# Optimization experiments

Measured on AMD Instinct MI355X. Metric: run time of the kernel, lower is better.

Reference implementation:

```python
import math
import jax, jax.numpy as jnp
import numpy as np

B, T, QDIM, ADIM = 256, 2048, 1024, 128
DC, DK = 8, 21          # dynamic channels / kernel
SC, SK = 8, 21          # static channels / kernel
PL, ALPHA, BETA = 11, 0.1, 0.9


def _betabinom_pmf_flipped(n, a, b, length):
    lg = np.vectorize(math.lgamma)
    k = np.arange(length, dtype=np.float64)
    logp = (lg(n + 1.0) - lg(k + 1.0) - lg(n - k + 1.0)
            + lg(k + a) + lg(n - k + b) - lg(n + a + b)
            - (lg(a) + lg(b) - lg(a + b)))
    return np.exp(logp)[::-1].copy()  # .flip(0) as in the torch buffer


def setup_inputs() -> dict:
    key = jax.random.key(0)
    ks = jax.random.split(key, 10)

    def lin(k, shape, fan_in):
        return (jax.random.normal(k, shape, jnp.float32) / np.sqrt(fan_in)).astype(jnp.float32)

    query = jax.random.normal(ks[0], (B, QDIM), jnp.float32)
    # previous-step alignment: a valid probability distribution over T
    alignment_pre = jax.nn.softmax(2.0 * jax.random.normal(ks[1], (B, T), jnp.float32), axis=1)

    P = jnp.asarray(_betabinom_pmf_flipped(PL - 1, ALPHA, BETA, PL), jnp.float32)
    W_w = lin(ks[2], (ADIM, QDIM), QDIM)
    W_b = jnp.zeros((ADIM,), jnp.float32)
    V_w = lin(ks[3], (DC * DK, ADIM), ADIM)
    F_w = lin(ks[4], (SC, 1, SK), SK)        # Conv1d(1, SC, SK) weight
    U_w = lin(ks[5], (ADIM, SC), SC)
    T_w = lin(ks[6], (ADIM, DC), DC)
    T_b = jnp.zeros((ADIM,), jnp.float32)
    v_w = lin(ks[7], (1, ADIM), ADIM)
    return {"query": query, "alignment_pre": alignment_pre, "P": P,
            "W_w": W_w, "W_b": W_b, "V_w": V_w, "F_w": F_w,
            "U_w": U_w, "T_w": T_w, "T_b": T_b, "v_w": v_w}


def reference(query, alignment_pre, P, W_w, W_b, V_w, F_w, U_w, T_w, T_b, v_w):
    b, t = alignment_pre.shape
    pad = (DK - 1) // 2  # == PL - 1 == 10, shared by all three convs
    x_pad = jnp.pad(alignment_pre, ((0, 0), (pad, pad)))
    # sliding windows (cross-correlation layout): windows[b, t, k] = x_pad[b, t + k]
    windows = jnp.stack([x_pad[:, k:k + t] for k in range(DK)], axis=-1)  # (B, T, DK)

    # prior: causal conv with left pad PL-1 == windows taps 0..PL-1
    p = jnp.log(jnp.clip(jnp.einsum('btk,k->bt', windows[..., :PL], P), 1e-6))

    # per-sample dynamic kernels
    G = jnp.tanh(query @ W_w.T + W_b) @ V_w.T          # (B, DC*DK)
    G = G.reshape(b, DC, DK)
    g = jnp.einsum('btk,bck->btc', windows, G)          # grouped conv, groups=B -> (B, T, DC)

    # static conv over previous alignment
    f = jnp.einsum('btk,ck->btc', windows, F_w[:, 0, :])  # (B, T, SC)

    e = jnp.squeeze(jnp.tanh(f @ U_w.T + g @ T_w.T + T_b) @ v_w.T, -1) + p  # (B, T)
    return jax.nn.softmax(e, axis=1)
```

## Files before the change

### kernel.cpp

```cpp
#include <hip/hip_runtime.h>
#include <hip/hip_bf16.h>

#define Bsz 256
#define Tn 2048
#define QD 1024
#define AD 128
#define DCn 8
#define DKn 21
#define PLn 11
#define GN (DCn * DKn)
#define XS2 24

typedef _Float16 f16x8 __attribute__((ext_vector_type(8)));
typedef float f32x4 __attribute__((ext_vector_type(4)));

#define TWO_LOG2E 2.8853900817779268f

__global__ __launch_bounds__(1024, 4) void dca_kernel(
    const float* __restrict__ query, const float* __restrict__ align,
    const float* __restrict__ P, const float* __restrict__ W_w,
    const float* __restrict__ W_b, const float* __restrict__ V_w,
    const float* __restrict__ F_w, const float* __restrict__ U_w,
    const float* __restrict__ T_w, const float* __restrict__ T_b,
    const float* __restrict__ v_w, float* __restrict__ out)
{
    __shared__ _Float16 al16[Tn + 44];
    __shared__ float    pcb[Tn];
    __shared__ float    sden[Tn];
    __shared__ _Float16 Xw[16 * 2 * 16 * XS2];
    __shared__ float    h_lds[AD];
    __shared__ float    G_lds[GN];
    __shared__ float    red[16];
    __shared__ float    bc;

    const int b    = blockIdx.x;
    const int tid  = threadIdx.x;
    const int lane = tid & 63;
    const int wid  = tid >> 6;
    const int l15  = lane & 15;
    const int quad = lane >> 4;

    for (int i = tid; i < Tn + 44; i += 1024) {
        int s = i - 10;
        float v = (s >= 0 && s < Tn) ? align[b * Tn + s] : 0.f;
        al16[i] = (_Float16)v;
    }

    {
        const float4* q4 = (const float4*)(query + b * QD);
        float4 q0 = q4[lane];
        float4 q1 = q4[64 + lane];
        float4 q2 = q4[128 + lane];
        float4 q3 = q4[192 + lane];
        #pragma unroll 2
        for (int i = 0; i < 8; ++i) {
            int a = wid * 8 + i;
            const float4* w4 = (const float4*)(W_w + a * QD);
            float4 x0 = w4[lane];
            float4 x1 = w4[64 + lane];
            float4 x2 = w4[128 + lane];
            float4 x3 = w4[192 + lane];
            float accA = 0.f, accB = 0.f;
            accA = fmaf(q0.x, x0.x, fmaf(q0.y, x0.y, fmaf(q0.z, x0.z, fmaf(q0.w, x0.w, accA))));
            accB = fmaf(q1.x, x1.x, fmaf(q1.y, x1.y, fmaf(q1.z, x1.z, fmaf(q1.w, x1.w, accB))));
            accA = fmaf(q2.x, x2.x, fmaf(q2.y, x2.y, fmaf(q2.z, x2.z, fmaf(q2.w, x2.w, accA))));
            accB = fmaf(q3.x, x3.x, fmaf(q3.y, x3.y, fmaf(q3.z, x3.z, fmaf(q3.w, x3.w, accB))));
            float acc = accA + accB;
            #pragma unroll
            for (int off = 32; off; off >>= 1) acc += __shfl_xor(acc, off);
            if (lane == 0) h_lds[a] = tanhf(acc + W_b[a]);
        }
    }
    __syncthreads();

    if (tid < GN) {
        float g = 0.f;
        #pragma unroll 4
        for (int i = 0; i < AD; ++i) g = fmaf(h_lds[i], V_w[tid * AD + i], g);
        G_lds[tid] = g;
    }

    const int t0w = wid * 128;
    #pragma unroll
    for (int tt = 0; tt < 2; ++tt) {
        int t = t0w + tt * 64 + lane;
        float pr = 0.f;
        #pragma unroll
        for (int k = 0; k < PLn; ++k) pr = fmaf((float)al16[t + k], P[k], pr);
        pcb[t] = fmaxf(pr, 1e-6f);
    }
    __syncthreads();

    f16x8 Bc = {};
    #pragma unroll
    for (int j = 0; j < 8; ++j) {
        int k = quad * 8 + j;
        float wv = 0.f;
        if (k < DKn) wv = (l15 < 8) ? F_w[l15 * DKn + k]
                                    : G_lds[(l15 - 8) * DKn + k];
        Bc[j] = (_Float16)wv;
    }

    f16x8 Bf[8];
    #pragma unroll
    for (int n = 0; n < 8; ++n) {
        int a = n * 16 + l15;
        f16x8 bf = {};
        if (quad < 2) {
            const float* src = (quad == 0) ? (U_w + a * 8) : (T_w + a * 8);
            float4 lo = ((const float4*)src)[0];
            float4 hi = ((const float4*)src)[1];
            bf[0] = (_Float16)(TWO_LOG2E * lo.x); bf[1] = (_Float16)(TWO_LOG2E * lo.y);
            bf[2] = (_Float16)(TWO_LOG2E * lo.z); bf[3] = (_Float16)(TWO_LOG2E * lo.w);
            bf[4] = (_Float16)(TWO_LOG2E * hi.x); bf[5] = (_Float16)(TWO_LOG2E * hi.y);
            bf[6] = (_Float16)(TWO_LOG2E * hi.z); bf[7] = (_Float16)(TWO_LOG2E * hi.w);
        } else if (quad == 2) {
            bf[0] = (_Float16)(TWO_LOG2E * T_b[a]);
        }
        Bf[n] = bf;
    }

    f32x4 vnq[8];
    float vsum = 0.f;
    #pragma unroll
    for (int n = 0; n < 8; ++n) {
        f32x4 vq = *(const f32x4*)(v_w + n * 16 + quad * 4);
        vsum += vq[0] + vq[1] + vq[2] + vq[3];
        vq[0] *= -2.f; vq[1] *= -2.f; vq[2] *= -2.f; vq[3] *= -2.f;
        vnq[n] = vq;
    }
    vsum += __shfl_xor(vsum, 16);
    vsum += __shfl_xor(vsum, 32);

    _Float16* Xp0 = &Xw[wid * 2 * 16 * XS2];
    _Float16* Xp1 = Xp0 + 16 * XS2;
    float wsum = 0.f;

    #pragma unroll 1
    for (int m = 0; m < 8; m += 2) {
        const int ta  = t0w + m * 16;
        const int tb_ = ta + 16;

        f16x8 Ac0, Ac1;
        #pragma unroll
        for (int j = 0; j < 8; ++j) {
            Ac0[j] = al16[ta  + l15 + quad * 8 + j];
            Ac1[j] = al16[tb_ + l15 + quad * 8 + j];
        }
        f32x4 z = {};
        f32x4 X0 = __builtin_amdgcn_mfma_f32_16x16x32_f16(Ac0, Bc, z, 0, 0, 0);
        f32x4 X1 = __builtin_amdgcn_mfma_f32_16x16x32_f16(Ac1, Bc, z, 0, 0, 0);

        #pragma unroll
        for (int r = 0; r < 4; ++r) {
            Xp0[(quad * 4 + r) * XS2 + l15] = (_Float16)X0[r];
            Xp1[(quad * 4 + r) * XS2 + l15] = (_Float16)X1[r];
        }
        __asm__ __volatile__("" ::: "memory");

        f16x8 B20 = {}, B21 = {};
        if (quad < 2) {
            B20 = *(const f16x8*)&Xp0[l15 * XS2 + quad * 8];
            B21 = *(const f16x8*)&Xp1[l15 * XS2 + quad * 8];
        } else if (quad == 2) {
            B20[0] = (_Float16)1.f;
            B21[0] = (_Float16)1.f;
        }

        float es0 = 0.f, es1 = 0.f;
        #pragma unroll
        for (int n = 0; n < 8; ++n) {
            f32x4 z2 = {};
            f32x4 d0 = __builtin_amdgcn_mfma_f32_16x16x32_f16(Bf[n], B20, z2, 0, 0, 0);
            f32x4 d1 = __builtin_amdgcn_mfma_f32_16x16x32_f16(Bf[n], B21, z2, 0, 0, 0);
            #pragma unroll
            for (int r = 0; r < 4; ++r) {
                float qa = __builtin_amdgcn_exp2f(d0[r]);
                float qb = __builtin_amdgcn_exp2f(d1[r]);
                float ra = __builtin_amdgcn_rcpf(qa + 1.f);
                float rb = __builtin_amdgcn_rcpf(qb + 1.f);
                es0 = fmaf(vnq[n][r], ra, es0);
                es1 = fmaf(vnq[n][r], rb, es1);
            }
        }
        es0 += __shfl_xor(es0, 16);
        es0 += __shfl_xor(es0, 32);
        es1 += __shfl_xor(es1, 16);
        es1 += __shfl_xor(es1, 32);

        if (lane < 16) {
            int tA = ta  + lane;
            int tB = tb_ + lane;
            float svA = pcb[tA] * __expf(es0 + vsum);
            float svB = pcb[tB] * __expf(es1 + vsum);
            sden[tA] = svA;
            sden[tB] = svB;
            wsum += svA + svB;
        }
    }

    __syncthreads();
    #pragma unroll
    for (int off = 32; off; off >>= 1) wsum += __shfl_xor(wsum, off);
    if (lane == 0) red[wid] = wsum;
    __syncthreads();
    if (wid == 0) {
        float ss = (lane < 16) ? red[lane] : 0.f;
        #pragma unroll
        for (int off = 8; off; off >>= 1) ss += __shfl_xor(ss, off);
        if (lane == 0) bc = ss;
    }
    __syncthreads();
    const float inv = 1.f / bc;
    out[b * Tn + tid]        = sden[tid] * inv;
    out[b * Tn + tid + 1024] = sden[tid + 1024] * inv;
}

extern "C" void kernel_launch(void* const* d_in, const int* in_sizes, int n_in,
                              void* d_out, int out_size, void* d_ws, size_t ws_size,
                              hipStream_t stream) {
    const float* query = (const float*)d_in[0];
    const float* align = (const float*)d_in[1];
    const float* P     = (const float*)d_in[2];
    const float* W_w   = (const float*)d_in[3];
    const float* W_b   = (const float*)d_in[4];
    const float* V_w   = (const float*)d_in[5];
    const float* F_w   = (const float*)d_in[6];
    const float* U_w   = (const float*)d_in[7];
    const float* T_w   = (const float*)d_in[8];
    const float* T_b   = (const float*)d_in[9];
    const float* v_w   = (const float*)d_in[10];
    float* out = (float*)d_out;

    dca_kernel<<<Bsz, 1024, 0, stream>>>(query, align, P, W_w, W_b, V_w,
                                         F_w, U_w, T_w, T_b, v_w, out);
}
```

Measured before the change: 107.7 us.

## Hoist dynamic-kernel GEMVs into a batched pre-kernel sharing weight loads

Moves the query→tanh→V_w projection that builds the per-sample dynamic conv kernels out of the main kernel into a separate pre-kernel. Each pre-kernel block handles 4 samples, so each W_w row load is reused across four batches and the V_w dot product uses float4 loads. The main kernel then reads its 168 G values from a workspace buffer (or from the output buffer if the workspace is too small). This cuts repeated W_w traffic from 256 blocks, but adds a second launch and a dependent global round-trip, and the pre-kernel runs only 64 blocks.

```diff
diff --git a/kernel.cpp b/kernel.cpp
--- a/kernel.cpp
+++ b/kernel.cpp
@@ -11,24 +11,95 @@
 #define GN (DCn * DKn)
 #define XS2 24
 
+#define ABLK 4
+#define NGBLK (Bsz / ABLK)
+
 typedef _Float16 f16x8 __attribute__((ext_vector_type(8)));
 typedef float f32x4 __attribute__((ext_vector_type(4)));
 
 #define TWO_LOG2E 2.8853900817779268f
 
+__global__ __launch_bounds__(1024, 4) void g_pre_kernel(
+    const float* __restrict__ query, const float* __restrict__ W_w,
+    const float* __restrict__ W_b, const float* __restrict__ V_w,
+    float* __restrict__ G_all)
+{
+    __shared__ float h_lds[ABLK][AD];
+
+    const int tid  = threadIdx.x;
+    const int lane = tid & 63;
+    const int wid  = tid >> 6;
+    const int b0   = blockIdx.x * ABLK;
+
+    float4 q[ABLK][4];
+    #pragma unroll
+    for (int bb = 0; bb < ABLK; ++bb) {
+        const float4* q4 = (const float4*)(query + (size_t)(b0 + bb) * QD);
+        #pragma unroll
+        for (int c = 0; c < 4; ++c) q[bb][c] = q4[c * 64 + lane];
+    }
+
+    #pragma unroll 1
+    for (int i = 0; i < 8; ++i) {
+        const int a = wid * 8 + i;
+        const float4* w4 = (const float4*)(W_w + (size_t)a * QD);
+        float4 w0 = w4[lane];
+        float4 w1 = w4[64 + lane];
+        float4 w2 = w4[128 + lane];
+        float4 w3 = w4[192 + lane];
+
+        float acc[ABLK];
+        #pragma unroll
+        for (int bb = 0; bb < ABLK; ++bb) {
+            float accA = 0.f, accB = 0.f;
+            accA = fmaf(q[bb][0].x, w0.x, fmaf(q[bb][0].y, w0.y, fmaf(q[bb][0].z, w0.z, fmaf(q[bb][0].w, w0.w, accA))));
+            accB = fmaf(q[bb][1].x, w1.x, fmaf(q[bb][1].y, w1.y, fmaf(q[bb][1].z, w1.z, fmaf(q[bb][1].w, w1.w, accB))));
+            accA = fmaf(q[bb][2].x, w2.x, fmaf(q[bb][2].y, w2.y, fmaf(q[bb][2].z, w2.z, fmaf(q[bb][2].w, w2.w, accA))));
+            accB = fmaf(q[bb][3].x, w3.x, fmaf(q[bb][3].y, w3.y, fmaf(q[bb][3].z, w3.z, fmaf(q[bb][3].w, w3.w, accB))));
+            acc[bb] = accA + accB;
+        }
+        #pragma unroll
+        for (int bb = 0; bb < ABLK; ++bb) {
+            float v = acc[bb];
+            #pragma unroll
+            for (int off = 32; off; off >>= 1) v += __shfl_xor(v, off);
+            acc[bb] = v;
+        }
+        if (lane == 0) {
+            const float wb = W_b[a];
+            #pragma unroll
+            for (int bb = 0; bb < ABLK; ++bb) h_lds[bb][a] = tanhf(acc[bb] + wb);
+        }
+    }
+    __syncthreads();
+
+    if (tid < ABLK * GN) {
+        const int bb = tid / GN;
+        const int r  = tid - bb * GN;
+        const float4* v4 = (const float4*)(V_w + (size_t)r * AD);
+        const float4* h4 = (const float4*)h_lds[bb];
+        float g = 0.f;
+        #pragma unroll 8
+        for (int i = 0; i < AD / 4; ++i) {
+            float4 vv = v4[i];
+            float4 hh = h4[i];
+            g = fmaf(vv.x, hh.x, fmaf(vv.y, hh.y, fmaf(vv.z, hh.z, fmaf(vv.w, hh.w, g))));
+        }
+        G_all[(size_t)(b0 + bb) * Tn + r] = g;
+    }
+}
+
 __global__ __launch_bounds__(1024, 4) void dca_kernel(
-    const float* __restrict__ query, const float* __restrict__ align,
-    const float* __restrict__ P, const float* __restrict__ W_w,
-    const float* __restrict__ W_b, const float* __restrict__ V_w,
+    const float* __restrict__ align, const float* __restrict__ P,
     const float* __restrict__ F_w, const float* __restrict__ U_w,
     const float* __restrict__ T_w, const float* __restrict__ T_b,
-    const float* __restrict__ v_w, float* __restrict__ out)
+    const float* __restrict__ v_w, const float* __restrict__ G_all,
+    float* __restrict__ out)
 {
     __shared__ _Float16 al16[Tn + 44];
     __shared__ float    pcb[Tn];
     __shared__ float    sden[Tn];
     __shared__ _Float16 Xw[16 * 2 * 16 * XS2];
-    __shared__ float    h_lds[AD];
     __shared__ float    G_lds[GN];
     __shared__ float    red[16];
     __shared__ float    bc;
@@ -46,39 +117,9 @@
         al16[i] = (_Float16)v;
     }
 
-    {
-        const float4* q4 = (const float4*)(query + b * QD);
-        float4 q0 = q4[lane];
-        float4 q1 = q4[64 + lane];
-        float4 q2 = q4[128 + lane];
-        float4 q3 = q4[192 + lane];
-        #pragma unroll 2
-        for (int i = 0; i < 8; ++i) {
-            int a = wid * 8 + i;
-            const float4* w4 = (const float4*)(W_w + a * QD);
-            float4 x0 = w4[lane];
-            float4 x1 = w4[64 + lane];
-            float4 x2 = w4[128 + lane];
-            float4 x3 = w4[192 + lane];
-            float accA = 0.f, accB = 0.f;
-            accA = fmaf(q0.x, x0.x, fmaf(q0.y, x0.y, fmaf(q0.z, x0.z, fmaf(q0.w, x0.w, accA))));
-            accB = fmaf(q1.x, x1.x, fmaf(q1.y, x1.y, fmaf(q1.z, x1.z, fmaf(q1.w, x1.w, accB))));
-            accA = fmaf(q2.x, x2.x, fmaf(q2.y, x2.y, fmaf(q2.z, x2.z, fmaf(q2.w, x2.w, accA))));
-            accB = fmaf(q3.x, x3.x, fmaf(q3.y, x3.y, fmaf(q3.z, x3.z, fmaf(q3.w, x3.w, accB))));
-            float acc = accA + accB;
-            #pragma unroll
-            for (int off = 32; off; off >>= 1) acc += __shfl_xor(acc, off);
-            if (lane == 0) h_lds[a] = tanhf(acc + W_b[a]);
-        }
-    }
-    __syncthreads();
-
-    if (tid < GN) {
-        float g = 0.f;
-        #pragma unroll 4
-        for (int i = 0; i < AD; ++i) g = fmaf(h_lds[i], V_w[tid * AD + i], g);
-        G_lds[tid] = g;
-    }
+    if (tid < GN) G_lds[tid] = G_all[(size_t)b * Tn + tid];
+
+    __syncthreads();
 
     const int t0w = wid * 128;
     #pragma unroll
@@ -89,7 +130,6 @@
         for (int k = 0; k < PLn; ++k) pr = fmaf((float)al16[t + k], P[k], pr);
         pcb[t] = fmaxf(pr, 1e-6f);
     }
-    __syncthreads();
 
     f16x8 Bc = {};
     #pragma unroll
@@ -232,6 +272,10 @@
     const float* v_w   = (const float*)d_in[10];
     float* out = (float*)d_out;
 
-    dca_kernel<<<Bsz, 1024, 0, stream>>>(query, align, P, W_w, W_b, V_w,
-                                         F_w, U_w, T_w, T_b, v_w, out);
+    float* Gbuf = (ws_size >= (size_t)Bsz * Tn * sizeof(float)) ? (float*)d_ws
+                                                                : out;
+
+    g_pre_kernel<<<NGBLK, 1024, 0, stream>>>(query, W_w, W_b, V_w, Gbuf);
+    dca_kernel<<<Bsz, 1024, 0, stream>>>(align, P, F_w, U_w, T_w, T_b, v_w,
+                                         Gbuf, out);
 }
```

Result: slower. 121.5 us (+12.8%).
